# Optimization experiments

Hardware: AMD Instinct MI355X
Metric: run time of the kernel (lower is better)

The kernel has to match this reference:

```python
import jax, jax.numpy as jnp
import numpy as np

P = 16
BN_EPS = 1e-5


def _to_patches(x, c, d):
    # [b, c*P, d*P] -> [b, c*d, P, P]
    b = x.shape[0]
    x = x.reshape(b, c, P, d, P).transpose(0, 1, 3, 2, 4)
    return x.reshape(b, c * d, P, P)


def _dwconv_block(x, dwk, g, bb, m, v, pwk):
    # depthwise 3x3 stride-2 conv (groups=C, no bias) + BN(eval) + GELU + 1x1 pointwise
    C = x.shape[1]
    y = jax.lax.conv_general_dilated(
        x, dwk[:, None, :, :], window_strides=(2, 2), padding=((1, 1), (1, 1)),
        feature_group_count=C, dimension_numbers=('NCHW', 'OIHW', 'NCHW'))
    y = g[None, :, None, None] * (y - m[None, :, None, None]) / jnp.sqrt(v + BN_EPS)[None, :, None, None] + bb[None, :, None, None]
    y = jax.nn.gelu(y, approximate=False)  # torch nn.GELU default = erf
    return jnp.einsum('bchw,oc->bohw', y, pwk)


def _forward(query, key, value, dw_k, bn_g, bn_b, bn_m, bn_v, pw_k, position, c1_w, c1_b, lin_w, lin_b):
    b, units, d_model = query.shape
    c = units // P
    d = d_model // P
    hp = P // 2  # spatial after stride-2 conv
    dk = hp * hp  # d_k = 64

    q = _to_patches(query, c, d)
    k = _to_patches(key, c, d)
    v = _to_patches(value, c, d)

    q = _dwconv_block(q, dw_k[0], bn_g[0], bn_b[0], bn_m[0], bn_v[0], pw_k[0])
    k = _dwconv_block(k, dw_k[1], bn_g[1], bn_b[1], bn_m[1], bn_v[1], pw_k[1])
    v = _dwconv_block(v, dw_k[2], bn_g[2], bn_b[2], bn_m[2], bn_v[2], pw_k[2])

    # [b, c*d, hp, hp] -> [b, c, d, hp*hp]
    q = q.reshape(b, c, d, dk)
    k = k.reshape(b, c, d, dk)
    v = v.reshape(b, c, d, dk)

    scores = jnp.einsum('bcdk,bcek->bcde', q, k) / jnp.sqrt(jnp.asarray(dk, q.dtype))
    scores = scores + position[None]  # learned additive position bias [c,d,d]
    p_attn = jax.nn.softmax(scores, axis=-1)
    x = jnp.einsum('bcde,bcek->bcdk', p_attn, v)  # [b, c, d, dk]

    # 'b c d (p1 p2) -> b (c p1) (d p2)', p1 = P//2
    x = x.reshape(b, c, d, hp, hp).transpose(0, 1, 3, 2, 4).reshape(b, c * hp, d * hp)

    # Conv1d(units//2 -> units, kernel 1) then Linear(d_model//2 -> d_model)
    x = jnp.einsum('bcl,oc->bol', x, c1_w) + c1_b[None, :, None]
    x = jnp.einsum('bcl,ol->bco', x, lin_w) + lin_b[None, None, :]
    return x


def setup_inputs() -> dict:
    key = jax.random.key(0)
    ks = jax.random.split(key, 8)
    b, units, d_model = 64, 32, 4096
    C = (units // P) * (d_model // P)  # 512
    inp = {
        'query': jax.random.normal(ks[0], (b, units, d_model), jnp.float32),
        'key': jax.random.normal(ks[1], (b, units, d_model), jnp.float32),
        'value': jax.random.normal(ks[2], (b, units, d_model), jnp.float32),
        'dw_k': jax.random.normal(ks[3], (3, C, 3, 3), jnp.float32) * 0.1,
        'bn_g': jnp.ones((3, C), jnp.float32),
        'bn_b': jnp.zeros((3, C), jnp.float32),
        'bn_m': jnp.zeros((3, C), jnp.float32),
        'bn_v': jnp.ones((3, C), jnp.float32),
        'pw_k': jax.random.normal(ks[4], (3, C, C), jnp.float32) * 0.02,
        'position': jax.random.normal(ks[5], (units // P, d_model // P, d_model // P), jnp.float32),
        'c1_w': jax.random.normal(ks[6], (units, units // 2), jnp.float32) * 0.1,
        'c1_b': jnp.zeros((units,), jnp.float32),
        'lin_w': jax.random.normal(ks[7], (d_model, d_model // 2), jnp.float32) * 0.02,
        'lin_b': jnp.zeros((d_model,), jnp.float32),
    }
    return inp


def reference(query, key, value, dw_k, bn_g, bn_b, bn_m, bn_v, pw_k, position, c1_w, c1_b, lin_w, lin_b):
    return _forward(query, key, value, dw_k, bn_g, bn_b, bn_m, bn_v, pw_k, position, c1_w, c1_b, lin_w, lin_b)
```

## Files before the change

### kernel.cpp

```cpp
#include <hip/hip_runtime.h>


typedef short s16x8 __attribute__((ext_vector_type(8)));
typedef float f32x4 __attribute__((ext_vector_type(4)));
typedef const __attribute__((address_space(1))) void* gas_t;
typedef __attribute__((address_space(3))) void* las_t;

__device__ __forceinline__ unsigned short f2bf(float x) {
  unsigned u = __float_as_uint(x);
  unsigned r = u + 0x7fffu + ((u >> 16) & 1u);
  return (unsigned short)(r >> 16);
}
__device__ __forceinline__ float bf2f(unsigned short h) {
  return __uint_as_float((unsigned)h << 16);
}

__global__ __launch_bounds__(256) void stageA_kernel(
    const float* __restrict__ xq, const float* __restrict__ xk,
    const float* __restrict__ xv, const float* __restrict__ dwk,
    const float* __restrict__ bng, const float* __restrict__ bnb,
    const float* __restrict__ bnm, const float* __restrict__ bnv,
    unsigned short* __restrict__ tTp)
{
  const int i  = blockIdx.y;
  const float* x = (i == 0) ? xq : (i == 1) ? xk : xv;
  const float* dwk_i = dwk + (size_t)i * 4608;
  const int co = i * 512;
  unsigned short* out = tTp + (size_t)i * 4194304;

  const int dd = threadIdx.x;
  const int oh = blockIdx.x & 7;
  const int cc = (blockIdx.x >> 3) & 1;
  const int b  = blockIdx.x >> 4;
  const int ch = cc * 256 + dd;

  float r[3][16];
#pragma unroll
  for (int kh = 0; kh < 3; ++kh) {
    int ih = 2 * oh - 1 + kh;
    if (ih >= 0 && ih <= 15) {
      const float* p = x + (size_t)(b * 32 + cc * 16 + ih) * 4096 + dd * 16;
#pragma unroll
      for (int jq = 0; jq < 4; ++jq)
        *(float4*)&r[kh][jq * 4] = *(const float4*)(p + jq * 4);
    } else {
#pragma unroll
      for (int j = 0; j < 16; ++j) r[kh][j] = 0.f;
    }
  }
  float w9[9];
#pragma unroll
  for (int j = 0; j < 9; ++j) w9[j] = dwk_i[ch * 9 + j];
  const float scale = bng[co + ch] / sqrtf(bnv[co + ch] + 1e-5f);
  const float shift = bnb[co + ch] - bnm[co + ch] * scale;

#pragma unroll
  for (int ow = 0; ow < 8; ++ow) {
    float acc = 0.f;
#pragma unroll
    for (int kh = 0; kh < 3; ++kh)
#pragma unroll
      for (int kw = 0; kw < 3; ++kw) {
        int iw = 2 * ow - 1 + kw;
        if (iw >= 0 && iw <= 15) acc = fmaf(r[kh][iw], w9[kh * 3 + kw], acc);
      }
    float y = acc * scale + shift;
    y = 0.5f * y * (1.f + erff(y * 0.70710678118654752f));
    unsigned short hi = f2bf(y);
    unsigned short lo = f2bf(y - bf2f(hi));
    size_t rowb = (size_t)(b * 64 + oh * 8 + ow) * 1024;
    out[rowb + ch] = hi;
    out[rowb + 512 + ch] = lo;
  }
}

__global__ __launch_bounds__(256) void split_kernel(
    const float* __restrict__ src, unsigned short* __restrict__ dst,
    int kshift, int total4)
{
  int i = blockIdx.x * 256 + threadIdx.x;
  if (i >= total4) return;
  size_t i4 = (size_t)i * 4;
  int K = 1 << kshift;
  int r = (int)(i4 >> kshift);
  int c = (int)(i4 & (size_t)(K - 1));
  float4 xv = *(const float4*)(src + i4);
  unsigned short h0 = f2bf(xv.x), h1 = f2bf(xv.y), h2 = f2bf(xv.z), h3 = f2bf(xv.w);
  unsigned short l0 = f2bf(xv.x - bf2f(h0)), l1 = f2bf(xv.y - bf2f(h1));
  unsigned short l2 = f2bf(xv.z - bf2f(h2)), l3 = f2bf(xv.w - bf2f(h3));
  unsigned short* dr = dst + (size_t)r * (K * 2) + c;
  uint2 hp, lp;
  hp.x = (unsigned)h0 | ((unsigned)h1 << 16);
  hp.y = (unsigned)h2 | ((unsigned)h3 << 16);
  lp.x = (unsigned)l0 | ((unsigned)l1 << 16);
  lp.y = (unsigned)l2 | ((unsigned)l3 << 16);
  *(uint2*)dr = hp;
  *(uint2*)(dr + K) = lp;
}

__global__ __launch_bounds__(256) void gemm_split_kernel(
    const unsigned short* __restrict__ Aall, const unsigned short* __restrict__ Ball,
    unsigned short* __restrict__ Call, int M, int N, int K)
{
  __shared__ unsigned short sA[4096];
  __shared__ unsigned short sB[8192];
  const int t = threadIdx.x;
  const int z = blockIdx.z;
  const unsigned short* A = Aall + (size_t)z * 524288;
  const unsigned short* B = Ball + (size_t)z * 4194304;
  unsigned short* Cq = Call + (size_t)z * 4194304;
  const int m0 = blockIdx.y * 64, n0 = blockIdx.x * 128;
  const int Kp = 3 * K, twoK = 2 * K, Km = K - 1;
  const int lane = t & 63;
  const int wv = t >> 6;
  const int colbase = wv * 32;
  const int h = lane & 15, g = lane >> 4;

  f32x4 acc[4][2];
#pragma unroll
  for (int mf = 0; mf < 4; ++mf)
#pragma unroll
    for (int nf = 0; nf < 2; ++nf)
      acc[mf][nf] = (f32x4){0.f, 0.f, 0.f, 0.f};

  int srow[4], sblk[4];
#pragma unroll
  for (int it = 0; it < 4; ++it) {
    int s = it * 256 + t;
    srow[it] = s >> 3;
    sblk[it] = (s & 7) ^ (srow[it] & 7);
  }
  const int ldsw = (t & 192) << 4;

  for (int k0 = 0; k0 < Kp; k0 += 64) {
    __syncthreads();
#pragma unroll
    for (int it = 0; it < 2; ++it) {
      int kp = k0 + sblk[it] * 8;
      int ac = (kp < twoK) ? (kp & Km) : (kp - K);
      const unsigned short* ga = A + (size_t)(m0 + srow[it]) * twoK + ac;
      __builtin_amdgcn_global_load_lds((gas_t)(const void*)ga,
          (las_t)(void*)((char*)sA + (it * 4096 + ldsw)), 16, 0, 0);
    }
#pragma unroll
    for (int it = 0; it < 4; ++it) {
      int kp = k0 + sblk[it] * 8;
      int bc = (kp < twoK) ? kp : (kp - twoK);
      const unsigned short* gb = B + (size_t)(n0 + srow[it]) * twoK + bc;
      __builtin_amdgcn_global_load_lds((gas_t)(const void*)gb,
          (las_t)(void*)((char*)sB + (it * 4096 + ldsw)), 16, 0, 0);
    }
    __syncthreads();

#pragma unroll
    for (int kk = 0; kk < 2; ++kk) {
      s16x8 af[4], bfr[2];
#pragma unroll
      for (int mf = 0; mf < 4; ++mf) {
        int arow = mf * 16 + h;
        int aoff = arow * 128 + (((kk * 4 + g) ^ (h & 7)) << 4);
        af[mf] = *(const s16x8*)((const char*)sA + aoff);
      }
#pragma unroll
      for (int nf = 0; nf < 2; ++nf) {
        int brow = colbase + nf * 16 + h;
        int boff = brow * 128 + (((kk * 4 + g) ^ (h & 7)) << 4);
        bfr[nf] = *(const s16x8*)((const char*)sB + boff);
      }
#pragma unroll
      for (int mf = 0; mf < 4; ++mf)
#pragma unroll
        for (int nf = 0; nf < 2; ++nf)
          acc[mf][nf] = __builtin_amdgcn_mfma_f32_16x16x32_bf16(
              af[mf], bfr[nf], acc[mf][nf], 0, 0, 0);
    }
  }

  if (z < 2) {
#pragma unroll
    for (int mf = 0; mf < 4; ++mf) {
      int mbase = m0 + mf * 16 + g * 4;
#pragma unroll
      for (int nf = 0; nf < 2; ++nf) {
        int n = n0 + colbase + nf * 16 + h;
        int bb = n >> 6, d = n & 63;
#pragma unroll
        for (int qq = 0; qq < 4; ++qq) {
          int m = mbase + qq;
          int cc = m >> 8;
          size_t rowb = ((size_t)(bb * 2 + cc) * 256 + (m & 255)) * 128;
          float vvv = acc[mf][nf][qq];
          unsigned short hi = f2bf(vvv);
          unsigned short lo = f2bf(vvv - bf2f(hi));
          Cq[rowb + d] = hi;
          Cq[rowb + 64 + d] = lo;
        }
      }
    }
  } else {
#pragma unroll
    for (int mf = 0; mf < 4; ++mf) {
      int mbase = m0 + mf * 16 + g * 4;
      int cc = mbase >> 8;
      int mc = mbase & 255;
#pragma unroll
      for (int nf = 0; nf < 2; ++nf) {
        int n = n0 + colbase + nf * 16 + h;
        int bb = n >> 6, d = n & 63;
        size_t rowb = ((size_t)(bb * 2 + cc) * 64 + d) * 512;
        ushort4 hv, lv;
        float v0 = acc[mf][nf][0], v1 = acc[mf][nf][1];
        float v2 = acc[mf][nf][2], v3 = acc[mf][nf][3];
        hv.x = f2bf(v0); hv.y = f2bf(v1); hv.z = f2bf(v2); hv.w = f2bf(v3);
        lv.x = f2bf(v0 - bf2f(hv.x)); lv.y = f2bf(v1 - bf2f(hv.y));
        lv.z = f2bf(v2 - bf2f(hv.z)); lv.w = f2bf(v3 - bf2f(hv.w));
        *(ushort4*)&Cq[rowb + mc] = hv;
        *(ushort4*)&Cq[rowb + 256 + mc] = lv;
      }
    }
  }
}

__global__ __launch_bounds__(512, 2) void gemm_pipe_kernel(
    const unsigned short* __restrict__ A, const unsigned short* __restrict__ B,
    float* __restrict__ C, const float* __restrict__ bias,
    int M, int N, int K)
{
  __shared__ unsigned short lds[73728];
  const int t = threadIdx.x;

  const int flat = blockIdx.y * 32 + blockIdx.x;
  const int xcd = flat & 7;
  const int ii = flat >> 3;
  const int mt = (xcd >> 2) * 4 + (ii >> 3);
  const int ntile = (xcd & 3) * 8 + (ii & 7);
  const int m0 = mt * 256;
  const int n0 = ntile * 128;

  const int twoK = 2 * K, Km = K - 1;
  const int nt = (3 * K) >> 6;

  const int lane = t & 63;
  const int wv = t >> 6;
  const int wm = wv & 3, wn = wv >> 2;
  const int h = lane & 15, g = lane >> 4;

  f32x4 acc[4][4];
#pragma unroll
  for (int mf = 0; mf < 4; ++mf)
#pragma unroll
    for (int nf = 0; nf < 4; ++nf)
      acc[mf][nf] = (f32x4){0.f, 0.f, 0.f, 0.f};

  int arow[4], ablk[4], brow[2], bblk[2];
#pragma unroll
  for (int it = 0; it < 4; ++it) {
    int s = it * 512 + t;
    arow[it] = s >> 3;
    ablk[it] = (t & 7) ^ (arow[it] & 7);
  }
#pragma unroll
  for (int it = 0; it < 2; ++it) {
    int s = it * 512 + t;
    brow[it] = s >> 3;
    bblk[it] = (t & 7) ^ (brow[it] & 7);
  }

  auto issueA = [&](int buf, int tt, int it) {
    int kp = tt * 64 + ablk[it] * 8;
    int ac = (kp < twoK) ? (kp & Km) : (kp - K);
    __builtin_amdgcn_global_load_lds(
        (gas_t)(const void*)(A + (size_t)(m0 + arow[it]) * twoK + ac),
        (las_t)(void*)((char*)lds + (buf * 49152 + it * 8192 + t * 16)), 16, 0, 0);
  };
  auto issueB = [&](int buf, int tt, int it) {
    int kp = tt * 64 + bblk[it] * 8;
    int bc = (kp < twoK) ? kp : (kp - twoK);
    __builtin_amdgcn_global_load_lds(
        (gas_t)(const void*)(B + (size_t)(n0 + brow[it]) * twoK + bc),
        (las_t)(void*)((char*)lds + (buf * 49152 + 32768 + it * 8192 + t * 16)), 16, 0, 0);
  };

  const int aoffb = (wm * 64 + h) * 128;
  const int boffb = 32768 + (wn * 64 + h) * 128;
  int colx[2];
  colx[0] = ((g) ^ (h & 7)) << 4;
  colx[1] = ((4 + g) ^ (h & 7)) << 4;

  auto rdA = [&](int buf, int kk, int mf) -> s16x8 {
    return *(const s16x8*)((const char*)lds + (buf * 49152 + aoffb + mf * 2048 + colx[kk]));
  };
  auto rdB = [&](int buf, int kk, int nf) -> s16x8 {
    return *(const s16x8*)((const char*)lds + (buf * 49152 + boffb + nf * 2048 + colx[kk]));
  };

#define MFMA_ROW2(A0, A1, A2, A3, BB, NF) \
  acc[0][NF] = __builtin_amdgcn_mfma_f32_16x16x32_bf16(A0, BB, acc[0][NF], 0, 0, 0); \
  acc[1][NF] = __builtin_amdgcn_mfma_f32_16x16x32_bf16(A1, BB, acc[1][NF], 0, 0, 0); \
  acc[2][NF] = __builtin_amdgcn_mfma_f32_16x16x32_bf16(A2, BB, acc[2][NF], 0, 0, 0); \
  acc[3][NF] = __builtin_amdgcn_mfma_f32_16x16x32_bf16(A3, BB, acc[3][NF], 0, 0, 0);

#pragma unroll
  for (int it = 0; it < 4; ++it) issueA(0, 0, it);
#pragma unroll
  for (int it = 0; it < 2; ++it) issueB(0, 0, it);
#pragma unroll
  for (int it = 0; it < 4; ++it) issueA(1, 1, it);
#pragma unroll
  for (int it = 0; it < 2; ++it) issueB(1, 1, it);
  asm volatile("s_waitcnt vmcnt(6)" ::: "memory");
  __builtin_amdgcn_sched_barrier(0);
  __builtin_amdgcn_s_barrier();
  __builtin_amdgcn_sched_barrier(0);

  int bR = 0;
  for (int tt = 0; tt <= nt - 3; ++tt) {
    const int bn2 = (bR >= 1) ? bR - 1 : 2;
    s16x8 a0 = rdA(bR, 0, 0), a1 = rdA(bR, 0, 1), a2 = rdA(bR, 0, 2), a3 = rdA(bR, 0, 3);
    s16x8 b0 = rdB(bR, 0, 0), b1 = rdB(bR, 0, 1), b2 = rdB(bR, 0, 2), b3 = rdB(bR, 0, 3);
    issueA(bn2, tt + 2, 0); issueA(bn2, tt + 2, 1);
    issueA(bn2, tt + 2, 2); issueA(bn2, tt + 2, 3);
    __builtin_amdgcn_s_barrier();
    __builtin_amdgcn_s_setprio(1);
    MFMA_ROW2(a0, a1, a2, a3, b0, 0)
    MFMA_ROW2(a0, a1, a2, a3, b1, 1)
    MFMA_ROW2(a0, a1, a2, a3, b2, 2)
    MFMA_ROW2(a0, a1, a2, a3, b3, 3)
    __builtin_amdgcn_s_setprio(0);
    __builtin_amdgcn_s_barrier();
    a0 = rdA(bR, 1, 0); a1 = rdA(bR, 1, 1); a2 = rdA(bR, 1, 2); a3 = rdA(bR, 1, 3);
    b0 = rdB(bR, 1, 0); b1 = rdB(bR, 1, 1); b2 = rdB(bR, 1, 2); b3 = rdB(bR, 1, 3);
    issueB(bn2, tt + 2, 0); issueB(bn2, tt + 2, 1);
    __builtin_amdgcn_s_barrier();
    __builtin_amdgcn_s_setprio(1);
    MFMA_ROW2(a0, a1, a2, a3, b0, 0)
    MFMA_ROW2(a0, a1, a2, a3, b1, 1)
    MFMA_ROW2(a0, a1, a2, a3, b2, 2)
    MFMA_ROW2(a0, a1, a2, a3, b3, 3)
    __builtin_amdgcn_s_setprio(0);
    asm volatile("s_waitcnt vmcnt(6)" ::: "memory");
    __builtin_amdgcn_sched_barrier(0);
    __builtin_amdgcn_s_barrier();
    __builtin_amdgcn_sched_barrier(0);
    bR = (bR == 2) ? 0 : bR + 1;
  }

  auto compute_tile = [&](int buf) {
#pragma unroll
    for (int kk = 0; kk < 2; ++kk) {
      s16x8 ta0 = rdA(buf, kk, 0), ta1 = rdA(buf, kk, 1);
      s16x8 ta2 = rdA(buf, kk, 2), ta3 = rdA(buf, kk, 3);
      s16x8 tb0 = rdB(buf, kk, 0), tb1 = rdB(buf, kk, 1);
      s16x8 tb2 = rdB(buf, kk, 2), tb3 = rdB(buf, kk, 3);
      MFMA_ROW2(ta0, ta1, ta2, ta3, tb0, 0)
      MFMA_ROW2(ta0, ta1, ta2, ta3, tb1, 1)
      MFMA_ROW2(ta0, ta1, ta2, ta3, tb2, 2)
      MFMA_ROW2(ta0, ta1, ta2, ta3, tb3, 3)
    }
  };
  compute_tile(bR);
  __syncthreads();
  compute_tile((bR == 2) ? 0 : bR + 1);
#undef MFMA_ROW2

#pragma unroll
  for (int mf = 0; mf < 4; ++mf) {
    int mbase = m0 + wm * 64 + mf * 16 + g * 4;
#pragma unroll
    for (int nf = 0; nf < 4; ++nf) {
      int n = n0 + wn * 64 + nf * 16 + h;
      float bv = bias[n];
#pragma unroll
      for (int qq = 0; qq < 4; ++qq)
        C[(size_t)(mbase + qq) * N + n] = acc[mf][nf][qq] + bv;
    }
  }
}

__global__ __launch_bounds__(256) void attn_mfma_kernel(
    const unsigned short* __restrict__ qp, const unsigned short* __restrict__ kp,
    const unsigned short* __restrict__ vtp, const float* __restrict__ pos,
    float* __restrict__ xatt)
{
  __shared__ char smem[59904];
  unsigned short* qs = (unsigned short*)smem;
  unsigned short* kv = (unsigned short*)(smem + 8704);
  float* sc = (float*)(smem + 26112);
  unsigned short* ps = (unsigned short*)(smem + 26112);

  const int t = threadIdx.x;
  const int rt = blockIdx.x, cc = blockIdx.y, b = blockIdx.z;
  const int i0 = rt * 32;
  const size_t qkbase = (size_t)(b * 2 + cc) * 256;
  const size_t vbase  = (size_t)(b * 2 + cc) * 64;

  const int lane = t & 63, wvv = t >> 6;
  const int h = lane & 15, g = lane >> 4;

#pragma unroll
  for (int rep = 0; rep < 2; ++rep) {
    int s = t + rep * 256;
    int row = s >> 4;
    int blk = s & 15;
    int4 val = *(const int4*)(qp + (qkbase + i0 + row) * 128 + blk * 8);
    *(int4*)((char*)qs + row * 272 + blk * 16) = val;
  }

  for (int c = 0; c < 4; ++c) {
    __syncthreads();
#pragma unroll
    for (int p2 = 0; p2 < 4; ++p2) {
      int s = t + p2 * 256;
      int row = s >> 4;
      int blk = s & 15;
      int4 val = *(const int4*)(kp + (qkbase + c * 64 + row) * 128 + blk * 8);
      *(int4*)((char*)kv + row * 272 + blk * 16) = val;
    }
    __syncthreads();
    f32x4 acc2[2];
    acc2[0] = (f32x4){0.f, 0.f, 0.f, 0.f};
    acc2[1] = (f32x4){0.f, 0.f, 0.f, 0.f};
#pragma unroll
    for (int kk = 0; kk < 6; ++kk) {
      int abase = (kk < 2) ? kk * 32 : (kk < 4) ? 64 + (kk - 2) * 32 : (kk - 4) * 32;
      int bbase = (kk < 2) ? kk * 32 : (kk < 4) ? (kk - 2) * 32 : 64 + (kk - 4) * 32;
      s16x8 bfrag = *(const s16x8*)((char*)kv + (wvv * 16 + h) * 272 + (bbase + g * 8) * 2);
#pragma unroll
      for (int mf = 0; mf < 2; ++mf) {
        s16x8 afrag = *(const s16x8*)((char*)qs + (mf * 16 + h) * 272 + (abase + g * 8) * 2);
        acc2[mf] = __builtin_amdgcn_mfma_f32_16x16x32_bf16(afrag, bfrag, acc2[mf], 0, 0, 0);
      }
    }
#pragma unroll
    for (int mf = 0; mf < 2; ++mf)
#pragma unroll
      for (int qq = 0; qq < 4; ++qq) {
        int row = mf * 16 + g * 4 + qq;
        int j = c * 64 + wvv * 16 + h;
        sc[row * 264 + j] = acc2[mf][qq] * 0.125f +
            pos[((size_t)cc * 256 + i0 + row) * 256 + j];
      }
  }
  __syncthreads();

  {
    const int r = t >> 3, j8 = t & 7;
    float e[32];
    float mx = -3.4e38f;
#pragma unroll
    for (int jj = 0; jj < 32; ++jj) {
      e[jj] = sc[r * 264 + j8 + 8 * jj];
      mx = fmaxf(mx, e[jj]);
    }
#pragma unroll
    for (int mset = 1; mset < 8; mset <<= 1) mx = fmaxf(mx, __shfl_xor(mx, mset, 64));
    float sum = 0.f;
#pragma unroll
    for (int jj = 0; jj < 32; ++jj) {
      e[jj] = expf(e[jj] - mx);
      sum += e[jj];
    }
#pragma unroll
    for (int mset = 1; mset < 8; mset <<= 1) sum += __shfl_xor(sum, mset, 64);
    float inv = 1.f / sum;
    __syncthreads();
#pragma unroll
    for (int jj = 0; jj < 32; ++jj) {
      float pv = e[jj] * inv;
      unsigned short hi = f2bf(pv);
      unsigned short lo = f2bf(pv - bf2f(hi));
      int j = j8 + 8 * jj;
      ps[r * 528 + j] = hi;
      ps[r * 528 + 264 + j] = lo;
    }
  }

  f32x4 oacc[2];
  oacc[0] = (f32x4){0.f, 0.f, 0.f, 0.f};
  oacc[1] = (f32x4){0.f, 0.f, 0.f, 0.f};
  for (int c = 0; c < 4; ++c) {
    __syncthreads();
#pragma unroll
    for (int p2 = 0; p2 < 4; ++p2) {
      int s = t + p2 * 256, row = s >> 4, blk = s & 15;
      int col = (blk < 8) ? (c * 64 + blk * 8) : (256 + c * 64 + (blk - 8) * 8);
      int4 val = *(const int4*)(vtp + (vbase + row) * 512 + col);
      *(int4*)((char*)kv + row * 272 + blk * 16) = val;
    }
    __syncthreads();
#pragma unroll
    for (int kk = 0; kk < 6; ++kk) {
      int abase = (kk < 2) ? (c * 64 + kk * 32)
                : (kk < 4) ? (264 + c * 64 + (kk - 2) * 32)
                           : (c * 64 + (kk - 4) * 32);
      int bbase = (kk < 2) ? kk * 32 : (kk < 4) ? (kk - 2) * 32 : 64 + (kk - 4) * 32;
      s16x8 bfrag = *(const s16x8*)((char*)kv + (wvv * 16 + h) * 272 + (bbase + g * 8) * 2);
#pragma unroll
      for (int mf = 0; mf < 2; ++mf) {
        s16x8 afrag = *(const s16x8*)((char*)ps + (mf * 16 + h) * 1056 + (abase + g * 8) * 2);
        oacc[mf] = __builtin_amdgcn_mfma_f32_16x16x32_bf16(afrag, bfrag, oacc[mf], 0, 0, 0);
      }
    }
  }
#pragma unroll
  for (int mf = 0; mf < 2; ++mf)
#pragma unroll
    for (int qq = 0; qq < 4; ++qq) {
      int row = mf * 16 + g * 4 + qq;
      int d = wvv * 16 + h;
      xatt[((size_t)(b * 2 + cc) * 256 + i0 + row) * 64 + d] = oacc[mf][qq];
    }
}

__global__ __launch_bounds__(512) void conv1d_kernel(
    const float* __restrict__ xatt, const float* __restrict__ w,
    const float* __restrict__ bias, unsigned short* __restrict__ y1p)
{
  __shared__ float X[16][520];
  __shared__ float W[512];
  __shared__ float Bp[32];
  const int t = threadIdx.x;
  const int lt = blockIdx.x;
  const int b  = blockIdx.y;
  if (t < 512) W[t] = w[t];
  if (t < 32) Bp[t] = bias[t];
#pragma unroll
  for (int cc = 0; cc < 2; ++cc) {
    const float* src = xatt + ((size_t)(b * 2 + cc) * 256 + lt * 64) * 64;
#pragma unroll
    for (int pass = 0; pass < 2; ++pass) {
      int f4 = t + pass * 512;
      float4 v4 = *(const float4*)(src + (size_t)f4 * 4);
      int fl = f4 * 4;
      int dl = fl >> 6;
      int rr = fl & 63;
      int p1 = rr >> 3, p2 = rr & 7;
      *(float4*)&X[cc * 8 + p1][dl * 8 + p2] = v4;
    }
  }
  __syncthreads();

  float xv[16];
#pragma unroll
  for (int ch = 0; ch < 16; ++ch) xv[ch] = X[ch][t];

  size_t obase = (size_t)b * 32 * 4096 + lt * 512 + t;
#pragma unroll
  for (int o = 0; o < 32; ++o) {
    float s = Bp[o];
#pragma unroll
    for (int ch = 0; ch < 16; ++ch) s = fmaf(xv[ch], W[o * 16 + ch], s);
    unsigned short hi = f2bf(s);
    unsigned short lo = f2bf(s - bf2f(hi));
    y1p[obase + (size_t)o * 4096] = hi;
    y1p[obase + (size_t)o * 4096 + 2048] = lo;
  }
}

extern "C" void kernel_launch(void* const* d_in, const int* in_sizes, int n_in,
                              void* d_out, int out_size, void* d_ws, size_t ws_size,
                              hipStream_t stream) {
  const float* q    = (const float*)d_in[0];
  const float* k    = (const float*)d_in[1];
  const float* v    = (const float*)d_in[2];
  const float* dwk  = (const float*)d_in[3];
  const float* bng  = (const float*)d_in[4];
  const float* bnb  = (const float*)d_in[5];
  const float* bnm  = (const float*)d_in[6];
  const float* bnv  = (const float*)d_in[7];
  const float* pwk  = (const float*)d_in[8];
  const float* pos  = (const float*)d_in[9];
  const float* c1w  = (const float*)d_in[10];
  const float* c1b  = (const float*)d_in[11];
  const float* linw = (const float*)d_in[12];
  const float* linb = (const float*)d_in[13];
  float* out = (float*)d_out;

  if (ws_size < 50331648u) return;

  char* ws = (char*)d_ws;
  unsigned short* qp   = (unsigned short*)(ws + 0);
  unsigned short* kpp  = (unsigned short*)(ws + 8388608);
  unsigned short* vtp  = (unsigned short*)(ws + 16777216);
  unsigned short* tTp  = (unsigned short*)(ws + 25165824);
  unsigned short* pwkp = (unsigned short*)d_out;
  float*          xatt = (float*)(ws + 25165824);
  unsigned short* y1p  = (unsigned short*)(ws + 0);
  unsigned short* lwp  = (unsigned short*)(ws + 16777216);

  split_kernel<<<768, 256, 0, stream>>>(pwk, pwkp, 9, 196608);

  stageA_kernel<<<dim3(1024, 3), 256, 0, stream>>>(
      q, k, v, dwk, bng, bnb, bnm, bnv, tTp);

  gemm_split_kernel<<<dim3(32, 8, 3), 256, 0, stream>>>(
      pwkp, tTp, qp, 512, 4096, 512);

  dim3 g2(8, 2, 64);
  attn_mfma_kernel<<<g2, 256, 0, stream>>>(qp, kpp, vtp, pos, xatt);

  conv1d_kernel<<<dim3(4, 64), 512, 0, stream>>>(xatt, c1w, c1b, y1p);

  split_kernel<<<8192, 256, 0, stream>>>(linw, lwp, 11, 2097152);

  dim3 g3(32, 8);
  gemm_pipe_kernel<<<g3, 512, 0, stream>>>(y1p, lwp, out, linb, 2048, 4096, 2048);
}
```

Measured before the change: 217.5 us.

## Reorder conv1d after linear GEMM to shrink the large GEMM's M dimension

Uses associativity to apply the Linear (d_model/2→d_model) GEMM first on the attention output with M=1024 instead of 2048, then applies the small 16→32 channel conv1d in an epilogue. The conv bias is folded in through the row sums of lin_w, computed with atomics during the split pass. The attention kernel now writes its output directly as a split hi/lo bf16 GEMM operand, which removes the separate conv1d pass and its fp32 round trip. In exchange it adds an fp32 intermediate G, an extra epilogue kernel and a memset, and it retiles the GEMM to a smaller 64x128 block.

After: 223.8 us. 2.9% more time.

```diff
diff --git a/kernel.cpp b/kernel.cpp
--- a/kernel.cpp
+++ b/kernel.cpp
@@ -98,6 +98,33 @@
   *(uint2*)(dr + K) = lp;
 }
 
+__global__ __launch_bounds__(256) void split_rs_kernel(
+    const float* __restrict__ src, unsigned short* __restrict__ dst,
+    float* __restrict__ rs, int total4)
+{
+  int i = blockIdx.x * 256 + threadIdx.x;
+  if (i >= total4) return;
+  size_t i4 = (size_t)i * 4;
+  int r = (int)(i4 >> 11);
+  int c = (int)(i4 & 2047);
+  float4 xv = *(const float4*)(src + i4);
+  unsigned short h0 = f2bf(xv.x), h1 = f2bf(xv.y), h2 = f2bf(xv.z), h3 = f2bf(xv.w);
+  unsigned short l0 = f2bf(xv.x - bf2f(h0)), l1 = f2bf(xv.y - bf2f(h1));
+  unsigned short l2 = f2bf(xv.z - bf2f(h2)), l3 = f2bf(xv.w - bf2f(h3));
+  unsigned short* dr = dst + (size_t)r * 4096 + c;
+  uint2 hp, lp;
+  hp.x = (unsigned)h0 | ((unsigned)h1 << 16);
+  hp.y = (unsigned)h2 | ((unsigned)h3 << 16);
+  lp.x = (unsigned)l0 | ((unsigned)l1 << 16);
+  lp.y = (unsigned)l2 | ((unsigned)l3 << 16);
+  *(uint2*)dr = hp;
+  *(uint2*)(dr + 2048) = lp;
+  float s = xv.x + xv.y + xv.z + xv.w;
+#pragma unroll
+  for (int off = 1; off < 64; off <<= 1) s += __shfl_xor(s, off, 64);
+  if ((threadIdx.x & 63) == 0) atomicAdd(&rs[r], s);
+}
+
 __global__ __launch_bounds__(256) void gemm_split_kernel(
     const unsigned short* __restrict__ Aall, const unsigned short* __restrict__ Ball,
     unsigned short* __restrict__ Call, int M, int N, int K)
@@ -221,49 +248,45 @@
   }
 }
 
-__global__ __launch_bounds__(512, 2) void gemm_pipe_kernel(
+__global__ __launch_bounds__(256, 2) void gemm_final_kernel(
     const unsigned short* __restrict__ A, const unsigned short* __restrict__ B,
-    float* __restrict__ C, const float* __restrict__ bias,
-    int M, int N, int K)
+    float* __restrict__ C, int M, int N, int K)
 {
-  __shared__ unsigned short lds[73728];
+  __shared__ unsigned short lds[36864];
   const int t = threadIdx.x;
 
   const int flat = blockIdx.y * 32 + blockIdx.x;
-  const int xcd = flat & 7;
-  const int ii = flat >> 3;
-  const int mt = (xcd >> 2) * 4 + (ii >> 3);
-  const int ntile = (xcd & 3) * 8 + (ii & 7);
-  const int m0 = mt * 256;
-  const int n0 = ntile * 128;
+  const int swz = (flat & 7) * 64 + (flat >> 3);
+  const int n0 = (swz & 31) * 128;
+  const int m0 = (swz >> 5) * 64;
 
   const int twoK = 2 * K, Km = K - 1;
   const int nt = (3 * K) >> 6;
 
   const int lane = t & 63;
   const int wv = t >> 6;
-  const int wm = wv & 3, wn = wv >> 2;
+  const int colbase = wv * 32;
   const int h = lane & 15, g = lane >> 4;
 
-  f32x4 acc[4][4];
+  f32x4 acc[4][2];
 #pragma unroll
   for (int mf = 0; mf < 4; ++mf)
 #pragma unroll
-    for (int nf = 0; nf < 4; ++nf)
+    for (int nf = 0; nf < 2; ++nf)
       acc[mf][nf] = (f32x4){0.f, 0.f, 0.f, 0.f};
 
-  int arow[4], ablk[4], brow[2], bblk[2];
+  int arow[2], ablk[2], brow[4], bblk[4];
+#pragma unroll
+  for (int it = 0; it < 2; ++it) {
+    int s = it * 256 + t;
+    arow[it] = s >> 3;
+    ablk[it] = (s & 7) ^ (arow[it] & 7);
+  }
 #pragma unroll
   for (int it = 0; it < 4; ++it) {
-    int s = it * 512 + t;
-    arow[it] = s >> 3;
-    ablk[it] = (t & 7) ^ (arow[it] & 7);
-  }
-#pragma unroll
-  for (int it = 0; it < 2; ++it) {
-    int s = it * 512 + t;
+    int s = it * 256 + t;
     brow[it] = s >> 3;
-    bblk[it] = (t & 7) ^ (brow[it] & 7);
+    bblk[it] = (s & 7) ^ (brow[it] & 7);
   }
 
   auto issueA = [&](int buf, int tt, int it) {
@@ -271,43 +294,47 @@
     int ac = (kp < twoK) ? (kp & Km) : (kp - K);
     __builtin_amdgcn_global_load_lds(
         (gas_t)(const void*)(A + (size_t)(m0 + arow[it]) * twoK + ac),
-        (las_t)(void*)((char*)lds + (buf * 49152 + it * 8192 + t * 16)), 16, 0, 0);
+        (las_t)(void*)((char*)lds + (buf * 24576 + it * 4096 + t * 16)), 16, 0, 0);
   };
   auto issueB = [&](int buf, int tt, int it) {
     int kp = tt * 64 + bblk[it] * 8;
     int bc = (kp < twoK) ? kp : (kp - twoK);
     __builtin_amdgcn_global_load_lds(
         (gas_t)(const void*)(B + (size_t)(n0 + brow[it]) * twoK + bc),
-        (las_t)(void*)((char*)lds + (buf * 49152 + 32768 + it * 8192 + t * 16)), 16, 0, 0);
+        (las_t)(void*)((char*)lds + (buf * 24576 + 8192 + it * 4096 + t * 16)), 16, 0, 0);
   };
 
-  const int aoffb = (wm * 64 + h) * 128;
-  const int boffb = 32768 + (wn * 64 + h) * 128;
   int colx[2];
   colx[0] = ((g) ^ (h & 7)) << 4;
   colx[1] = ((4 + g) ^ (h & 7)) << 4;
 
   auto rdA = [&](int buf, int kk, int mf) -> s16x8 {
-    return *(const s16x8*)((const char*)lds + (buf * 49152 + aoffb + mf * 2048 + colx[kk]));
+    return *(const s16x8*)((const char*)lds +
+        (buf * 24576 + (mf * 16 + h) * 128 + colx[kk]));
   };
   auto rdB = [&](int buf, int kk, int nf) -> s16x8 {
-    return *(const s16x8*)((const char*)lds + (buf * 49152 + boffb + nf * 2048 + colx[kk]));
+    return *(const s16x8*)((const char*)lds +
+        (buf * 24576 + 8192 + (colbase + nf * 16 + h) * 128 + colx[kk]));
   };
 
-#define MFMA_ROW2(A0, A1, A2, A3, BB, NF) \
-  acc[0][NF] = __builtin_amdgcn_mfma_f32_16x16x32_bf16(A0, BB, acc[0][NF], 0, 0, 0); \
-  acc[1][NF] = __builtin_amdgcn_mfma_f32_16x16x32_bf16(A1, BB, acc[1][NF], 0, 0, 0); \
-  acc[2][NF] = __builtin_amdgcn_mfma_f32_16x16x32_bf16(A2, BB, acc[2][NF], 0, 0, 0); \
-  acc[3][NF] = __builtin_amdgcn_mfma_f32_16x16x32_bf16(A3, BB, acc[3][NF], 0, 0, 0);
-
-#pragma unroll
-  for (int it = 0; it < 4; ++it) issueA(0, 0, it);
-#pragma unroll
-  for (int it = 0; it < 2; ++it) issueB(0, 0, it);
-#pragma unroll
-  for (int it = 0; it < 4; ++it) issueA(1, 1, it);
-#pragma unroll
-  for (int it = 0; it < 2; ++it) issueB(1, 1, it);
+#define MFMA8(A0, A1, A2, A3, B0, B1) \
+  acc[0][0] = __builtin_amdgcn_mfma_f32_16x16x32_bf16(A0, B0, acc[0][0], 0, 0, 0); \
+  acc[1][0] = __builtin_amdgcn_mfma_f32_16x16x32_bf16(A1, B0, acc[1][0], 0, 0, 0); \
+  acc[2][0] = __builtin_amdgcn_mfma_f32_16x16x32_bf16(A2, B0, acc[2][0], 0, 0, 0); \
+  acc[3][0] = __builtin_amdgcn_mfma_f32_16x16x32_bf16(A3, B0, acc[3][0], 0, 0, 0); \
+  acc[0][1] = __builtin_amdgcn_mfma_f32_16x16x32_bf16(A0, B1, acc[0][1], 0, 0, 0); \
+  acc[1][1] = __builtin_amdgcn_mfma_f32_16x16x32_bf16(A1, B1, acc[1][1], 0, 0, 0); \
+  acc[2][1] = __builtin_amdgcn_mfma_f32_16x16x32_bf16(A2, B1, acc[2][1], 0, 0, 0); \
+  acc[3][1] = __builtin_amdgcn_mfma_f32_16x16x32_bf16(A3, B1, acc[3][1], 0, 0, 0);
+
+#pragma unroll
+  for (int it = 0; it < 2; ++it) issueA(0, 0, it);
+#pragma unroll
+  for (int it = 0; it < 4; ++it) issueB(0, 0, it);
+#pragma unroll
+  for (int it = 0; it < 2; ++it) issueA(1, 1, it);
+#pragma unroll
+  for (int it = 0; it < 4; ++it) issueB(1, 1, it);
   asm volatile("s_waitcnt vmcnt(6)" ::: "memory");
   __builtin_amdgcn_sched_barrier(0);
   __builtin_amdgcn_s_barrier();
@@ -317,26 +344,19 @@
   for (int tt = 0; tt <= nt - 3; ++tt) {
     const int bn2 = (bR >= 1) ? bR - 1 : 2;
     s16x8 a0 = rdA(bR, 0, 0), a1 = rdA(bR, 0, 1), a2 = rdA(bR, 0, 2), a3 = rdA(bR, 0, 3);
-    s16x8 b0 = rdB(bR, 0, 0), b1 = rdB(bR, 0, 1), b2 = rdB(bR, 0, 2), b3 = rdB(bR, 0, 3);
-    issueA(bn2, tt + 2, 0); issueA(bn2, tt + 2, 1);
-    issueA(bn2, tt + 2, 2); issueA(bn2, tt + 2, 3);
+    s16x8 b0 = rdB(bR, 0, 0), b1 = rdB(bR, 0, 1);
+    issueA(bn2, tt + 2, 0); issueA(bn2, tt + 2, 1); issueB(bn2, tt + 2, 0);
     __builtin_amdgcn_s_barrier();
     __builtin_amdgcn_s_setprio(1);
-    MFMA_ROW2(a0, a1, a2, a3, b0, 0)
-    MFMA_ROW2(a0, a1, a2, a3, b1, 1)
-    MFMA_ROW2(a0, a1, a2, a3, b2, 2)
-    MFMA_ROW2(a0, a1, a2, a3, b3, 3)
+    MFMA8(a0, a1, a2, a3, b0, b1)
     __builtin_amdgcn_s_setprio(0);
     __builtin_amdgcn_s_barrier();
     a0 = rdA(bR, 1, 0); a1 = rdA(bR, 1, 1); a2 = rdA(bR, 1, 2); a3 = rdA(bR, 1, 3);
-    b0 = rdB(bR, 1, 0); b1 = rdB(bR, 1, 1); b2 = rdB(bR, 1, 2); b3 = rdB(bR, 1, 3);
-    issueB(bn2, tt + 2, 0); issueB(bn2, tt + 2, 1);
+    b0 = rdB(bR, 1, 0); b1 = rdB(bR, 1, 1);
+    issueB(bn2, tt + 2, 1); issueB(bn2, tt + 2, 2); issueB(bn2, tt + 2, 3);
     __builtin_amdgcn_s_barrier();
     __builtin_amdgcn_s_setprio(1);
-    MFMA_ROW2(a0, a1, a2, a3, b0, 0)
-    MFMA_ROW2(a0, a1, a2, a3, b1, 1)
-    MFMA_ROW2(a0, a1, a2, a3, b2, 2)
-    MFMA_ROW2(a0, a1, a2, a3, b3, 3)
+    MFMA8(a0, a1, a2, a3, b0, b1)
     __builtin_amdgcn_s_setprio(0);
     asm volatile("s_waitcnt vmcnt(6)" ::: "memory");
     __builtin_amdgcn_sched_barrier(0);
@@ -351,28 +371,23 @@
       s16x8 ta0 = rdA(buf, kk, 0), ta1 = rdA(buf, kk, 1);
       s16x8 ta2 = rdA(buf, kk, 2), ta3 = rdA(buf, kk, 3);
       s16x8 tb0 = rdB(buf, kk, 0), tb1 = rdB(buf, kk, 1);
-      s16x8 tb2 = rdB(buf, kk, 2), tb3 = rdB(buf, kk, 3);
-      MFMA_ROW2(ta0, ta1, ta2, ta3, tb0, 0)
-      MFMA_ROW2(ta0, ta1, ta2, ta3, tb1, 1)
-      MFMA_ROW2(ta0, ta1, ta2, ta3, tb2, 2)
-      MFMA_ROW2(ta0, ta1, ta2, ta3, tb3, 3)
+      MFMA8(ta0, ta1, ta2, ta3, tb0, tb1)
     }
   };
   compute_tile(bR);
   __syncthreads();
   compute_tile((bR == 2) ? 0 : bR + 1);
-#undef MFMA_ROW2
+#undef MFMA8
 
 #pragma unroll
   for (int mf = 0; mf < 4; ++mf) {
-    int mbase = m0 + wm * 64 + mf * 16 + g * 4;
-#pragma unroll
-    for (int nf = 0; nf < 4; ++nf) {
-      int n = n0 + wn * 64 + nf * 16 + h;
-      float bv = bias[n];
+    int mbase = m0 + mf * 16 + g * 4;
+#pragma unroll
+    for (int nf = 0; nf < 2; ++nf) {
+      int n = n0 + colbase + nf * 16 + h;
 #pragma unroll
       for (int qq = 0; qq < 4; ++qq)
-        C[(size_t)(mbase + qq) * N + n] = acc[mf][nf][qq] + bv;
+        C[(size_t)(mbase + qq) * N + n] = acc[mf][nf][qq];
     }
   }
 }
@@ -380,7 +395,7 @@
 __global__ __launch_bounds__(256) void attn_mfma_kernel(
     const unsigned short* __restrict__ qp, const unsigned short* __restrict__ kp,
     const unsigned short* __restrict__ vtp, const float* __restrict__ pos,
-    float* __restrict__ xatt)
+    unsigned short* __restrict__ Xp)
 {
   __shared__ char smem[59904];
   unsigned short* qs = (unsigned short*)smem;
@@ -502,58 +517,51 @@
       }
     }
   }
-#pragma unroll
-  for (int mf = 0; mf < 2; ++mf)
-#pragma unroll
-    for (int qq = 0; qq < 4; ++qq) {
-      int row = mf * 16 + g * 4 + qq;
-      int d = wvv * 16 + h;
-      xatt[((size_t)(b * 2 + cc) * 256 + i0 + row) * 64 + d] = oacc[mf][qq];
-    }
-}
-
-__global__ __launch_bounds__(512) void conv1d_kernel(
-    const float* __restrict__ xatt, const float* __restrict__ w,
-    const float* __restrict__ bias, unsigned short* __restrict__ y1p)
+  {
+    int Xrow = b * 16 + cc * 8 + wvv * 2 + (h >> 3);
+    int c7 = h & 7;
+#pragma unroll
+    for (int mf = 0; mf < 2; ++mf)
+#pragma unroll
+      for (int qq = 0; qq < 4; ++qq) {
+        int dd = i0 + mf * 16 + g * 4 + qq;
+        float vvv = oacc[mf][qq];
+        unsigned short hi = f2bf(vvv);
+        unsigned short lo = f2bf(vvv - bf2f(hi));
+        size_t base = (size_t)Xrow * 4096 + dd * 8 + c7;
+        Xp[base] = hi;
+        Xp[base + 2048] = lo;
+      }
+  }
+}
+
+__global__ __launch_bounds__(256) void epilogue_kernel(
+    const float* __restrict__ G, const float* __restrict__ rs,
+    const float* __restrict__ c1w, const float* __restrict__ c1b,
+    const float* __restrict__ linb, float* __restrict__ out)
 {
-  __shared__ float X[16][520];
   __shared__ float W[512];
   __shared__ float Bp[32];
   const int t = threadIdx.x;
-  const int lt = blockIdx.x;
-  const int b  = blockIdx.y;
-  if (t < 512) W[t] = w[t];
-  if (t < 32) Bp[t] = bias[t];
-#pragma unroll
-  for (int cc = 0; cc < 2; ++cc) {
-    const float* src = xatt + ((size_t)(b * 2 + cc) * 256 + lt * 64) * 64;
-#pragma unroll
-    for (int pass = 0; pass < 2; ++pass) {
-      int f4 = t + pass * 512;
-      float4 v4 = *(const float4*)(src + (size_t)f4 * 4);
-      int fl = f4 * 4;
-      int dl = fl >> 6;
-      int rr = fl & 63;
-      int p1 = rr >> 3, p2 = rr & 7;
-      *(float4*)&X[cc * 8 + p1][dl * 8 + p2] = v4;
-    }
-  }
+  const int ntile = blockIdx.x;
+  const int b = blockIdx.y;
+  W[t] = c1w[t];
+  W[t + 256] = c1w[t + 256];
+  if (t < 32) Bp[t] = c1b[t];
   __syncthreads();
-
-  float xv[16];
-#pragma unroll
-  for (int ch = 0; ch < 16; ++ch) xv[ch] = X[ch][t];
-
-  size_t obase = (size_t)b * 32 * 4096 + lt * 512 + t;
+  const int n = ntile * 256 + t;
+  float gv[16];
+#pragma unroll
+  for (int ch = 0; ch < 16; ++ch)
+    gv[ch] = G[(size_t)(b * 16 + ch) * 4096 + n];
+  const float rsn = rs[n];
+  const float lbn = linb[n];
 #pragma unroll
   for (int o = 0; o < 32; ++o) {
-    float s = Bp[o];
-#pragma unroll
-    for (int ch = 0; ch < 16; ++ch) s = fmaf(xv[ch], W[o * 16 + ch], s);
-    unsigned short hi = f2bf(s);
-    unsigned short lo = f2bf(s - bf2f(hi));
-    y1p[obase + (size_t)o * 4096] = hi;
-    y1p[obase + (size_t)o * 4096 + 2048] = lo;
+    float s = lbn + Bp[o] * rsn;
+#pragma unroll
+    for (int ch = 0; ch < 16; ++ch) s = fmaf(W[o * 16 + ch], gv[ch], s);
+    out[(size_t)(b * 32 + o) * 4096 + n] = s;
   }
 }
 
@@ -584,9 +592,10 @@
   unsigned short* vtp  = (unsigned short*)(ws + 16777216);
   unsigned short* tTp  = (unsigned short*)(ws + 25165824);
   unsigned short* pwkp = (unsigned short*)d_out;
-  float*          xatt = (float*)(ws + 25165824);
-  unsigned short* y1p  = (unsigned short*)(ws + 0);
-  unsigned short* lwp  = (unsigned short*)(ws + 16777216);
+  unsigned short* Xp   = (unsigned short*)(ws + 25165824);
+  float*          rs   = (float*)(ws + 0);
+  unsigned short* lwp  = (unsigned short*)d_out;
+  float*          G    = (float*)(ws + 33554432);
 
   split_kernel<<<768, 256, 0, stream>>>(pwk, pwkp, 9, 196608);
 
@@ -596,13 +605,12 @@
   gemm_split_kernel<<<dim3(32, 8, 3), 256, 0, stream>>>(
       pwkp, tTp, qp, 512, 4096, 512);
 
-  dim3 g2(8, 2, 64);
-  attn_mfma_kernel<<<g2, 256, 0, stream>>>(qp, kpp, vtp, pos, xatt);
-
-  conv1d_kernel<<<dim3(4, 64), 512, 0, stream>>>(xatt, c1w, c1b, y1p);
-
-  split_kernel<<<8192, 256, 0, stream>>>(linw, lwp, 11, 2097152);
-
-  dim3 g3(32, 8);
-  gemm_pipe_kernel<<<g3, 512, 0, stream>>>(y1p, lwp, out, linb, 2048, 4096, 2048);
-}
+  attn_mfma_kernel<<<dim3(8, 2, 64), 256, 0, stream>>>(qp, kpp, vtp, pos, Xp);
+
+  hipMemsetAsync(rs, 0, 16384, stream);
+  split_rs_kernel<<<8192, 256, 0, stream>>>(linw, lwp, rs, 2097152);
+
+  gemm_final_kernel<<<dim3(32, 16), 256, 0, stream>>>(Xp, lwp, G, 1024, 4096, 2048);
+
+  epilogue_kernel<<<dim3(16, 64), 256, 0, stream>>>(G, rs, c1w, c1b, linb, out);
+}
```
